# Performance work log

Measured on AMD Instinct MI355X. Metric: run time of the kernel, lower is better.

Reference implementation:

```python
import jax, jax.numpy as jnp
import numpy as np

# Model dims (see init_kwargs)
B, S, D = 2, 2048, 2048          # batch, seq, hidden
H, HD = 16, 128                  # heads, head_dim (= ND + RD)
ND, RD = 64, 64                  # nope dim, rope dim per head
R = 512                          # kv lora rank
THETA = 10000.0


def _rotate_half(x):
    # interleaved rotation: pairs (x0,x1) -> (-x1, x0)
    x1 = x[..., ::2]
    x2 = x[..., 1::2]
    return jnp.stack((-x2, x1), axis=-1).reshape(x.shape)


def apply_rope(x, positions):
    # x: [..., seq, dim]
    dim = x.shape[-1]
    freqs = 1.0 / THETA ** (jnp.arange(0, dim, 2, dtype=x.dtype) / dim)  # [dim/2]
    angles = positions.astype(x.dtype)[:, None] * freqs                  # [seq, dim/2]
    cos = jnp.repeat(jnp.cos(angles), 2, axis=-1)[None, None]            # [1,1,seq,dim]
    sin = jnp.repeat(jnp.sin(angles), 2, axis=-1)[None, None]
    return x * cos + _rotate_half(x) * sin


def setup_inputs() -> dict:
    key = jax.random.key(0)
    ks = jax.random.split(key, 7)
    def lin(k, out_f, in_f):  # torch Linear convention: weight [out, in]
        return jax.random.normal(k, (out_f, in_f), dtype=jnp.float32) * (in_f ** -0.5)
    return {
        "x": jax.random.normal(ks[0], (B, S, D), dtype=jnp.float32),
        "wq": lin(ks[1], D, D),
        "w_kv_down": lin(ks[2], R, D),
        "w_k_up": lin(ks[3], H * ND, R),
        "w_k_rope": lin(ks[4], RD, D),
        "w_v_up": lin(ks[5], D, R),
        "wo": lin(ks[6], D, D),
    }


def reference(x, wq, w_kv_down, w_k_up, w_k_rope, w_v_up, wo):
    b, s, _ = x.shape
    pos = jnp.arange(s)
    scale = 1.0 / np.sqrt(HD).astype(np.float32)

    # queries: [b,H,s,HD] split into nope/rope parts, rope applied per head
    q = (x @ wq.T).reshape(b, s, H, HD).transpose(0, 2, 1, 3)
    q_nope = q[..., :ND]
    q_rope = apply_rope(q[..., ND:], pos)

    # compressed kv latent: [b,s,R]
    c_kv = x @ w_kv_down.T
    k_nope = (c_kv @ w_k_up.T).reshape(b, s, H, ND).transpose(0, 2, 1, 3)  # [b,H,s,ND]
    k_rope = apply_rope((x @ w_k_rope.T)[:, None], pos)[:, 0]             # [b,s,RD], shared across heads
    v = (c_kv @ w_v_up.T).reshape(b, s, H, HD).transpose(0, 2, 1, 3)      # [b,H,s,HD]

    # decomposed scores: nope part (per head) + rope part (shared k)
    scores = jnp.einsum('bhqd,bhkd->bhqk', q_nope, k_nope)
    scores = scores + jnp.einsum('bhqd,bkd->bhqk', q_rope, k_rope)
    scores = scores * scale

    causal = jnp.tril(jnp.ones((s, s), dtype=bool))
    scores = jnp.where(causal[None, None], scores, jnp.finfo(scores.dtype).min)
    attn = jax.nn.softmax(scores, axis=-1)

    out = jnp.einsum('bhqk,bhkd->bhqd', attn, v)
    out = out.transpose(0, 2, 1, 3).reshape(b, s, D)
    return out @ wo.T
```

## Files before the change

kernel.cpp:

```cpp
#include <hip/hip_runtime.h>
#include <stdint.h>


typedef unsigned short u16;
typedef __bf16 bf16x8 __attribute__((ext_vector_type(8)));
typedef float f32x4 __attribute__((ext_vector_type(4)));

#define QLD 2816

__device__ __forceinline__ float bf2f(u16 u) {
    union { unsigned int i; float f; } x; x.i = ((unsigned int)u) << 16; return x.f;
}
__device__ __forceinline__ u16 f2bf(float f) {
    union { float f; unsigned int i; } x; x.f = f;
    unsigned int r = x.i + 0x7fffu + ((x.i >> 16) & 1u);
    return (u16)(r >> 16);
}
__device__ __forceinline__ void store_c(u16* p, float v)  { *p = f2bf(v); }
__device__ __forceinline__ void store_c(float* p, float v){ *p = v; }

#define GLOBAL_AS __attribute__((address_space(1)))
#define LDS_AS    __attribute__((address_space(3)))
__device__ __forceinline__ void gl_lds16(const void* g, void* l) {
    __builtin_amdgcn_global_load_lds((GLOBAL_AS const void*)g, (LDS_AS void*)l, 16, 0, 0);
}

#if __has_builtin(__builtin_amdgcn_exp2f)
__device__ __forceinline__ float exp2fast(float x) { return __builtin_amdgcn_exp2f(x); }
#else
__device__ __forceinline__ float exp2fast(float x) { return __expf(x * 0.6931471805599453f); }
#endif

template<int CTRL>
__device__ __forceinline__ float fmax_dpp(float v) {
    int s = __builtin_bit_cast(int, v);
    int t = __builtin_amdgcn_update_dpp(s, s, CTRL, 0xF, 0xF, true);
    return fmaxf(v, __builtin_bit_cast(float, t));
}
__device__ __forceinline__ float rowmax16(float v) {
    v = fmax_dpp<0xB1>(v);
    v = fmax_dpp<0x4E>(v);
    v = fmax_dpp<0x124>(v);
    v = fmax_dpp<0x128>(v);
    return v;
}

__device__ __forceinline__ void cv8(const float* __restrict__ src,
                                    u16* __restrict__ dst, int i) {
    const float4* s = (const float4*)src;
    float4 v0 = s[2*i], v1 = s[2*i + 1];
    union { u16 u[8]; uint4 v; } o;
    o.u[0] = f2bf(v0.x); o.u[1] = f2bf(v0.y); o.u[2] = f2bf(v0.z); o.u[3] = f2bf(v0.w);
    o.u[4] = f2bf(v1.x); o.u[5] = f2bf(v1.y); o.u[6] = f2bf(v1.z); o.u[7] = f2bf(v1.w);
    *((uint4*)(dst + 8*i)) = o.v;
}

__global__ void convert_all(const float* __restrict__ s_x,
                            const float* __restrict__ s_wq,
                            const float* __restrict__ s_kvd,
                            const float* __restrict__ s_kup,
                            const float* __restrict__ s_vup,
                            const float* __restrict__ s_kr,
                            u16* __restrict__ xc, u16* __restrict__ wqcat,
                            u16* __restrict__ kupc, u16* __restrict__ vupc) {
    int i = blockIdx.x * 256 + threadIdx.x;
    if      (i < 1048576) cv8(s_x,   xc,                          i);
    else if (i < 1572864) cv8(s_wq,  wqcat,                       i - 1048576);
    else if (i < 1703936) cv8(s_kvd, wqcat + (size_t)2112*2048,   i - 1572864);
    else if (i < 1769472) cv8(s_kup, kupc,                        i - 1703936);
    else if (i < 1900544) cv8(s_vup, vupc,                        i - 1769472);
    else if (i < 1916928) cv8(s_kr,  wqcat + (size_t)2048*2048,   i - 1900544);
}

template<int BM, int BN, int EPI, typename CT>
__global__ __launch_bounds__((BM/64)*(BN/64)*64)
void gemm_bt(const u16* __restrict__ A, const u16* __restrict__ W,
             CT* __restrict__ C, int M, int N, int K,
             int lda, int ldw, int ldc) {
    constexpr int BK = 32;
    constexpr int NWAVE = (BM/64)*(BN/64);
    constexpr int NT = NWAVE * 64;
    __shared__ u16 As[BM*BK];
    __shared__ u16 Bs[BN*BK];
    const int tid  = threadIdx.x;
    const int lane = tid & 63, l15 = lane & 15, quad = lane >> 4;
    const int wave = tid >> 6;
    const int wm = wave % (BM/64);
    const int wn = wave / (BM/64);
    const int bm = blockIdx.y * BM;
    const int bn = blockIdx.x * BN;

    const f32x4 fzero = {0.f, 0.f, 0.f, 0.f};
    f32x4 acc[4][4];
    #pragma unroll
    for (int i = 0; i < 4; ++i)
        #pragma unroll
        for (int j = 0; j < 4; ++j) acc[i][j] = fzero;

    const size_t Ab = (size_t)lda * 2;
    const size_t Wb = (size_t)ldw * 2;

    for (int k0 = 0; k0 < K; k0 += BK) {
        #pragma unroll
        for (int i = 0; i < (BM*64)/(NT*16); ++i) {
            int o = (tid + i*NT) * 16;
            int row = o >> 6, colb = o & 63;
            gl_lds16((const char*)A + (size_t)(bm + row)*Ab + (size_t)k0*2 + colb,
                     (char*)As + o);
        }
        #pragma unroll
        for (int i = 0; i < (BN*64)/(NT*16); ++i) {
            int o = (tid + i*NT) * 16;
            int row = o >> 6, colb = o & 63;
            gl_lds16((const char*)W + (size_t)(bn + row)*Wb + (size_t)k0*2 + colb,
                     (char*)Bs + o);
        }
        __syncthreads();

        bf16x8 af[4], bfv[4];
        #pragma unroll
        for (int mt = 0; mt < 4; ++mt)
            af[mt] = *reinterpret_cast<const bf16x8*>(&As[(wm*64 + mt*16 + l15)*BK + quad*8]);
        #pragma unroll
        for (int nt = 0; nt < 4; ++nt)
            bfv[nt] = *reinterpret_cast<const bf16x8*>(&Bs[(wn*64 + nt*16 + l15)*BK + quad*8]);
        #pragma unroll
        for (int mt = 0; mt < 4; ++mt)
            #pragma unroll
            for (int nt = 0; nt < 4; ++nt)
                acc[mt][nt] = __builtin_amdgcn_mfma_f32_16x16x32_bf16(
                    af[mt], bfv[nt], acc[mt][nt], 0, 0, 0);
        __syncthreads();
    }

    #pragma unroll
    for (int mt = 0; mt < 4; ++mt)
        #pragma unroll
        for (int nt = 0; nt < 4; ++nt)
            #pragma unroll
            for (int r = 0; r < 4; ++r) {
                int gm = bm + wm*64 + mt*16 + quad*4 + r;
                int gn = bn + wn*64 + nt*16 + l15;
                size_t ci;
                if (EPI == 1) ci = (size_t)gm*ldc + ((gn >> 6)*128 + (gn & 63));
                else          ci = (size_t)gm*ldc + gn;
                store_c(&C[ci], acc[mt][nt][r]);
            }
}

template<typename CT>
__global__ __launch_bounds__(512, 2)
void gemm256(const u16* __restrict__ A, const u16* __restrict__ W,
             CT* __restrict__ C, int K, int lda, int ldw, int ldc) {
    __shared__ u16 lds[4][16384];
    const int tid  = threadIdx.x;
    const int lane = tid & 63, l15 = lane & 15, quad = lane >> 4;
    const int wave = tid >> 6;
    const int wr = wave >> 2, wc = wave & 3;
    const int bm = blockIdx.y * 256;
    const int bn = blockIdx.x * 256;

    const int R = tid >> 2, slot = tid & 3;
    const int k16 = slot ^ ((R >> 1) & 3);
    const u16* asrc = A + (size_t)(bm + R) * lda + k16 * 8;
    const u16* bsrc = W + (size_t)(bn + R) * ldw + k16 * 8;
    const size_t astep = (size_t)128 * lda;
    const size_t bstep = (size_t)128 * ldw;

    #define STAGE256(st, bi) { \
        const u16* a0_ = asrc + (size_t)(st) * 32; \
        const u16* b0_ = bsrc + (size_t)(st) * 32; \
        gl_lds16(a0_,         &lds[bi][tid * 8]); \
        gl_lds16(a0_ + astep, &lds[bi][(tid + 512) * 8]); \
        gl_lds16(b0_,         &lds[bi][(tid + 1024) * 8]); \
        gl_lds16(b0_ + bstep, &lds[bi][(tid + 1536) * 8]); \
    }

    const f32x4 fzero = {0.f, 0.f, 0.f, 0.f};
    f32x4 acc[8][4];
    #pragma unroll
    for (int i = 0; i < 8; ++i)
        #pragma unroll
        for (int j = 0; j < 4; ++j) acc[i][j] = fzero;

    const int aswz = (quad ^ ((l15 >> 1) & 3)) * 8;

    const int nst = K >> 5;
    STAGE256(0, 0)
    STAGE256(1, 1)
    STAGE256(2, 2)
    asm volatile("s_waitcnt vmcnt(8)" ::: "memory");
    __builtin_amdgcn_s_barrier();

    for (int t = 0; t < nst; ++t) {
        const u16* buf = lds[t & 3];
        bf16x8 af[8], bfv[4];
        #pragma unroll
        for (int mf = 0; mf < 8; ++mf)
            af[mf] = *reinterpret_cast<const bf16x8*>(
                &buf[(wr*128 + mf*16 + l15)*32 + aswz]);
        #pragma unroll
        for (int nf = 0; nf < 4; ++nf)
            bfv[nf] = *reinterpret_cast<const bf16x8*>(
                &buf[8192 + (wc*64 + nf*16 + l15)*32 + aswz]);
        int st = t + 3; if (st > nst - 1) st = nst - 1;
        STAGE256(st, (t + 3) & 3)
        __builtin_amdgcn_s_setprio(1);
        #pragma unroll
        for (int mf = 0; mf < 8; ++mf)
            #pragma unroll
            for (int nf = 0; nf < 4; ++nf)
                acc[mf][nf] = __builtin_amdgcn_mfma_f32_16x16x32_bf16(
                    af[mf], bfv[nf], acc[mf][nf], 0, 0, 0);
        __builtin_amdgcn_s_setprio(0);
        asm volatile("s_waitcnt vmcnt(8) lgkmcnt(0)" ::: "memory");
        __builtin_amdgcn_sched_barrier(0);
        __builtin_amdgcn_s_barrier();
        __builtin_amdgcn_sched_barrier(0);
    }
    #undef STAGE256

    #pragma unroll
    for (int mf = 0; mf < 8; ++mf)
        #pragma unroll
        for (int nf = 0; nf < 4; ++nf)
            #pragma unroll
            for (int r = 0; r < 4; ++r) {
                int gm = bm + wr*128 + mf*16 + quad*4 + r;
                int gn = bn + wc*64 + nf*16 + l15;
                store_c(&C[(size_t)gm * ldc + gn], acc[mf][nf][r]);
            }
}

template<typename CT>
__global__ __launch_bounds__(512, 4)
void gemm128(const u16* __restrict__ A, const u16* __restrict__ W,
             CT* __restrict__ C, int K, int lda, int ldw, int ldc) {
    __shared__ u16 lds[3][12288];
    const int tid  = threadIdx.x;
    const int lane = tid & 63, l15 = lane & 15, quad = lane >> 4;
    const int wave = tid >> 6;
    const int wr = wave >> 2, wc = wave & 3;
    const int bm = blockIdx.y * 128;
    const int bn = blockIdx.x * 256;

    const int R = tid >> 2, slot = tid & 3;
    const int k16 = slot ^ ((R >> 1) & 3);
    const u16* asrc = A + (size_t)(bm + R) * lda + k16 * 8;
    const u16* bsrc = W + (size_t)(bn + R) * ldw + k16 * 8;
    const size_t bstep = (size_t)128 * ldw;

    #define STAGE128(st, bi) { \
        const u16* a0_ = asrc + (size_t)(st) * 32; \
        const u16* b0_ = bsrc + (size_t)(st) * 32; \
        gl_lds16(a0_,         &lds[bi][tid * 8]); \
        gl_lds16(b0_,         &lds[bi][(tid + 512) * 8]); \
        gl_lds16(b0_ + bstep, &lds[bi][(tid + 1024) * 8]); \
    }

    const f32x4 fzero = {0.f, 0.f, 0.f, 0.f};
    f32x4 acc[4][4];
    #pragma unroll
    for (int i = 0; i < 4; ++i)
        #pragma unroll
        for (int j = 0; j < 4; ++j) acc[i][j] = fzero;

    const int aswz = (quad ^ ((l15 >> 1) & 3)) * 8;

    const int nst = K >> 5;
    STAGE128(0, 0)
    STAGE128(1, 1)
    asm volatile("s_waitcnt vmcnt(3)" ::: "memory");
    __builtin_amdgcn_s_barrier();

    int b0 = 0, bs = 2;
    for (int t = 0; t < nst; ++t) {
        const u16* buf = lds[b0];
        bf16x8 af[4], bfv[4];
        #pragma unroll
        for (int mf = 0; mf < 4; ++mf)
            af[mf] = *reinterpret_cast<const bf16x8*>(
                &buf[(wr*64 + mf*16 + l15)*32 + aswz]);
        #pragma unroll
        for (int nf = 0; nf < 4; ++nf)
            bfv[nf] = *reinterpret_cast<const bf16x8*>(
                &buf[4096 + (wc*64 + nf*16 + l15)*32 + aswz]);
        int st = t + 2; if (st > nst - 1) st = nst - 1;
        STAGE128(st, bs)
        __builtin_amdgcn_s_setprio(1);
        #pragma unroll
        for (int mf = 0; mf < 4; ++mf)
            #pragma unroll
            for (int nf = 0; nf < 4; ++nf)
                acc[mf][nf] = __builtin_amdgcn_mfma_f32_16x16x32_bf16(
                    af[mf], bfv[nf], acc[mf][nf], 0, 0, 0);
        __builtin_amdgcn_s_setprio(0);
        asm volatile("s_waitcnt vmcnt(3) lgkmcnt(0)" ::: "memory");
        __builtin_amdgcn_sched_barrier(0);
        __builtin_amdgcn_s_barrier();
        __builtin_amdgcn_sched_barrier(0);
        b0 = (b0 == 2) ? 0 : b0 + 1;
        bs = (bs == 2) ? 0 : bs + 1;
    }
    #undef STAGE128

    #pragma unroll
    for (int mf = 0; mf < 4; ++mf)
        #pragma unroll
        for (int nf = 0; nf < 4; ++nf)
            #pragma unroll
            for (int r = 0; r < 4; ++r) {
                int gm = bm + wr*64 + mf*16 + quad*4 + r;
                int gn = bn + wc*64 + nf*16 + l15;
                store_c(&C[(size_t)gm * ldc + gn], acc[mf][nf][r]);
            }
}

__global__ void rope_woc(u16* __restrict__ qcat, u16* __restrict__ keff,
                         const float* __restrict__ wo_src, u16* __restrict__ woc) {
    const int blk = blockIdx.x;
    if (blk >= 512) {
        int i = (blk - 512) * 256 + threadIdx.x;
        cv8(wo_src, woc, i);
        return;
    }
    int idx = blk * 256 + threadIdx.x;
    int i = idx & 31, r = idx >> 5;
    int pos = r & 2047;
    float freq = powf(10000.0f, -(float)i * (1.0f/32.0f));
    float ang  = (float)pos * freq;
    float s = sinf(ang), c = cosf(ang);

    u16* row = qcat + (size_t)r * QLD + 64 + 2*i;
    #pragma unroll
    for (int h = 0; h < 16; ++h) {
        unsigned int* p = (unsigned int*)(row + h*128);
        unsigned int v = *p;
        float x0 = bf2f((u16)(v & 0xffffu)), x1 = bf2f((u16)(v >> 16));
        unsigned int lo = f2bf(x0*c - x1*s);
        unsigned int hi = f2bf(x1*c + x0*s);
        *p = lo | (hi << 16);
    }

    const u16* p = qcat + (size_t)r * QLD + 2048 + 2*i;
    float x0 = bf2f(p[0]), x1 = bf2f(p[1]);
    union { u16 u[2]; unsigned int w; } o;
    o.u[0] = f2bf(x0*c - x1*s);
    o.u[1] = f2bf(x1*c + x0*s);
    unsigned int* base = (unsigned int*)(keff + (size_t)r*2048 + 64 + 2*i);
    #pragma unroll
    for (int h = 0; h < 16; ++h) base[h*64] = o.w;
}

__global__ __launch_bounds__(256, 3)
void attn_kernel(u16* __restrict__ qcat, const u16* __restrict__ KE,
                 const u16* __restrict__ VT) {
    constexpr int S = 2048;
    const int L = (int)blockIdx.y * 16 + (int)blockIdx.x;
    const int xcd = L & 7, j = L >> 3;
    const int bh   = xcd * 4 + (j & 3);
    const int pair = j >> 2;
    const int b = bh >> 4, h = bh & 15;

    __shared__ u16 Ks[64*128];
    __shared__ u16 Vs[128*64];
    __shared__ u16 Ps[64*68];

    const int tid  = threadIdx.x;
    const int lane = tid & 63, l15 = lane & 15, quad = lane >> 4;
    const int wave = tid >> 6;

    const u16* ksrc[4];
    const u16* vsrc[4];
    #pragma unroll
    for (int i = 0; i < 4; ++i) {
        int g = tid + i*256;
        {
            int r = g >> 4, slot = g & 15, cg = slot ^ (r & 15);
            ksrc[i] = KE + (size_t)(b*S + r)*2048 + h*128 + cg*8;
        }
        {
            int d = g >> 3, slot = g & 7, cg = slot ^ (d & 7);
            vsrc[i] = VT + (size_t)(h*128 + d)*4096 + (size_t)(b*S) + cg*8;
        }
    }

    bf16x8 kreg[4], vreg[4];
    #pragma unroll
    for (int i = 0; i < 4; ++i) {
        kreg[i] = *reinterpret_cast<const bf16x8*>(ksrc[i]);
        vreg[i] = *reinterpret_cast<const bf16x8*>(vsrc[i]);
    }

    union { u16 u[8]; bf16x8 v; } onesu;
    #pragma unroll
    for (int i = 0; i < 8; ++i) onesu.u[i] = 0x3f80;
    const bf16x8 ones = onesu.v;

    const f32x4 fzero = {0.f, 0.f, 0.f, 0.f};
    const float NEG = -1e30f;
    const float KLOG = 0.12751739f;
    const float THR = 8.0f;

    __bf16* PsB = reinterpret_cast<__bf16*>(Ps);

    for (int half = 0; half < 2; ++half) {
        const int qt = half ? pair : 31 - pair;
        const int nkt = qt + 1;

        u16* qbase = qcat + (size_t)(b*S + qt*64) * QLD + h*128;
        bf16x8 aq[4];
        #pragma unroll
        for (int ks = 0; ks < 4; ++ks)
            aq[ks] = *reinterpret_cast<const bf16x8*>(
                qbase + (size_t)(wave*16 + l15)*QLD + ks*32 + quad*8);

        float m2[4]  = {NEG, NEG, NEG, NEG};
        float l_i[4] = {0.f, 0.f, 0.f, 0.f};
        f32x4 oacc[8];
        #pragma unroll
        for (int i = 0; i < 8; ++i) oacc[i] = fzero;

        const int qrow0 = qt*64 + wave*16 + quad*4;

        for (int kt = 0; kt < nkt; ++kt) {
            const bool is_last = (kt == nkt - 1);
            #pragma unroll
            for (int i = 0; i < 4; ++i) {
                *reinterpret_cast<bf16x8*>(&Ks[(tid + i*256) * 8]) = kreg[i];
                *reinterpret_cast<bf16x8*>(&Vs[(tid + i*256) * 8]) = vreg[i];
            }
            {
                int ktn = (kt + 1 < nkt) ? kt + 1 : 0;
                #pragma unroll
                for (int i = 0; i < 4; ++i) {
                    kreg[i] = *reinterpret_cast<const bf16x8*>(ksrc[i] + (size_t)ktn*(64*2048));
                    vreg[i] = *reinterpret_cast<const bf16x8*>(vsrc[i] + (size_t)ktn*64);
                }
            }
            __syncthreads();

            f32x4 sfr[4];
            __builtin_amdgcn_s_setprio(1);
            #pragma unroll
            for (int nt = 0; nt < 4; ++nt) {
                f32x4 s = fzero;
                int n = nt*16 + l15;
                #pragma unroll
                for (int ks = 0; ks < 4; ++ks) {
                    int c = ks*4 + quad;
                    bf16x8 bk = *reinterpret_cast<const bf16x8*>(&Ks[n*128 + ((c ^ l15) * 8)]);
                    s = __builtin_amdgcn_mfma_f32_16x16x32_bf16(aq[ks], bk, s, 0, 0, 0);
                }
                sfr[nt] = s;
            }
            __builtin_amdgcn_s_setprio(0);
            if (is_last) {
                #pragma unroll
                for (int nt = 0; nt < 4; ++nt) {
                    int kg = kt*64 + nt*16 + l15;
                    #pragma unroll
                    for (int r = 0; r < 4; ++r)
                        if (kg > qrow0 + r) sfr[nt][r] = NEG;
                }
            }
            float rm[4];
            #pragma unroll
            for (int r = 0; r < 4; ++r) {
                rm[r] = fmaxf(fmaxf(sfr[0][r], sfr[1][r]), fmaxf(sfr[2][r], sfr[3][r]));
                rm[r] = rowmax16(rm[r]);
            }
            float c2[4];
            int need = 0;
            #pragma unroll
            for (int r = 0; r < 4; ++r) {
                c2[r] = rm[r] * KLOG;
                need |= (c2[r] > m2[r] + THR) ? 1 : 0;
            }
            if (__any(need)) {
                float alpha[4];
                #pragma unroll
                for (int r = 0; r < 4; ++r) {
                    float mn = fmaxf(m2[r], c2[r]);
                    alpha[r] = exp2fast(m2[r] - mn);
                    m2[r] = mn;
                    l_i[r] *= alpha[r];
                }
                #pragma unroll
                for (int i = 0; i < 8; ++i)
                    #pragma unroll
                    for (int r = 0; r < 4; ++r)
                        oacc[i][r] *= alpha[r];
            }
            float pf[4][4];
            #pragma unroll
            for (int nt = 0; nt < 4; ++nt)
                #pragma unroll
                for (int r = 0; r < 4; ++r)
                    pf[nt][r] = exp2fast(__builtin_fmaf(sfr[nt][r], KLOG, -m2[r]));

            #pragma unroll
            for (int nt = 0; nt < 4; ++nt) {
                int base = (wave*16 + quad*4)*68 + nt*16 + l15;
                #pragma unroll
                for (int r = 0; r < 4; ++r)
                    PsB[base + r*68] = (__bf16)pf[nt][r];
            }

            f32x4 lfr = fzero;
            __builtin_amdgcn_s_setprio(1);
            #pragma unroll
            for (int ks = 0; ks < 2; ++ks) {
                bf16x8 pa = *reinterpret_cast<const bf16x8*>(
                    &Ps[(wave*16 + l15)*68 + ks*32 + quad*8]);
                lfr = __builtin_amdgcn_mfma_f32_16x16x32_bf16(pa, ones, lfr, 0, 0, 0);
                #pragma unroll
                for (int ntv = 0; ntv < 8; ++ntv) {
                    int c = ks*4 + quad;
                    bf16x8 bv = *reinterpret_cast<const bf16x8*>(
                        &Vs[(ntv*16 + l15)*64 + ((c ^ (l15 & 7)) * 8)]);
                    oacc[ntv] = __builtin_amdgcn_mfma_f32_16x16x32_bf16(pa, bv, oacc[ntv], 0, 0, 0);
                }
            }
            __builtin_amdgcn_s_setprio(0);
            #pragma unroll
            for (int r = 0; r < 4; ++r) l_i[r] += lfr[r];
            __syncthreads();
        }

        #pragma unroll
        for (int r = 0; r < 4; ++r) {
            float inv = 1.0f / l_i[r];
            int qrow = wave*16 + quad*4 + r;
            #pragma unroll
            for (int ntv = 0; ntv < 8; ++ntv) {
                int d = ntv*16 + l15;
                qbase[(size_t)qrow*QLD + d] = f2bf(oacc[ntv][r] * inv);
            }
        }
    }
}

extern "C" void kernel_launch(void* const* d_in, const int* in_sizes, int n_in,
                              void* d_out, int out_size, void* d_ws, size_t ws_size,
                              hipStream_t stream) {
    (void)in_sizes; (void)n_in; (void)out_size; (void)ws_size;
    float* out = (float*)d_out;
    char* ws = (char*)d_ws;

    u16* xc     = (u16*)(ws);
    u16* qcat   = (u16*)(ws + 16777216);
    u16* keff   = (u16*)(ws + 39845888);
    u16* wqcat  = (u16*)(ws + 56623104);
    u16* kupc   = (u16*)(ws + 68157440);
    u16* vupc   = (u16*)(ws + 69206016);
    u16* vT     = xc;
    u16* woc    = wqcat;

    convert_all<<<7488, 256, 0, stream>>>(
        (const float*)d_in[0], (const float*)d_in[1], (const float*)d_in[2],
        (const float*)d_in[3], (const float*)d_in[5], (const float*)d_in[4],
        xc, wqcat, kupc, vupc);

    gemm256<u16><<<dim3(11, 16), 512, 0, stream>>>(
        xc, wqcat, qcat, 2048, 2048, 2048, QLD);

    rope_woc<<<2560, 256, 0, stream>>>(qcat, keff, (const float*)d_in[6], woc);

    gemm_bt<128,128,1><<<dim3(8, 32), 256, 0, stream>>>(
        qcat + 2112, kupc, keff, 4096, 1024, 512, QLD, 512, 2048);

    gemm128<u16><<<dim3(16, 16), 512, 0, stream>>>(
        vupc, qcat + 2112, vT, 512, 512, QLD, 4096);

    attn_kernel<<<dim3(16, 32), 256, 0, stream>>>(qcat, keff, vT);

    gemm128<float><<<dim3(8, 32), 512, 0, stream>>>(
        qcat, woc, out, 2048, QLD, 2048, 2048);
}
```

Before: 315.2 us.

## Merge k_up and v_up GEMMs into one launch using pipelined gemm128 body

Replaces the simple unpipelined gemm_bt used for the k_nope up-projection with the pipelined gemm128 body, which gains a strided epilogue option. Both up-projection GEMMs (k_up into keff and v_up into vT) now run as one kernel with 384 blocks split by block index. This removes a launch and the tail between the two GEMMs, and the k GEMM gets the faster multi-buffered mainloop. The cost is that each k block now covers a 128x256 tile, so that part runs as fewer, larger blocks.

```diff
diff --git a/kernel.cpp b/kernel.cpp
--- a/kernel.cpp
+++ b/kernel.cpp
@@ -72,82 +72,6 @@
     else if (i < 1916928) cv8(s_kr,  wqcat + (size_t)2048*2048,   i - 1900544);
 }
 
-template<int BM, int BN, int EPI, typename CT>
-__global__ __launch_bounds__((BM/64)*(BN/64)*64)
-void gemm_bt(const u16* __restrict__ A, const u16* __restrict__ W,
-             CT* __restrict__ C, int M, int N, int K,
-             int lda, int ldw, int ldc) {
-    constexpr int BK = 32;
-    constexpr int NWAVE = (BM/64)*(BN/64);
-    constexpr int NT = NWAVE * 64;
-    __shared__ u16 As[BM*BK];
-    __shared__ u16 Bs[BN*BK];
-    const int tid  = threadIdx.x;
-    const int lane = tid & 63, l15 = lane & 15, quad = lane >> 4;
-    const int wave = tid >> 6;
-    const int wm = wave % (BM/64);
-    const int wn = wave / (BM/64);
-    const int bm = blockIdx.y * BM;
-    const int bn = blockIdx.x * BN;
-
-    const f32x4 fzero = {0.f, 0.f, 0.f, 0.f};
-    f32x4 acc[4][4];
-    #pragma unroll
-    for (int i = 0; i < 4; ++i)
-        #pragma unroll
-        for (int j = 0; j < 4; ++j) acc[i][j] = fzero;
-
-    const size_t Ab = (size_t)lda * 2;
-    const size_t Wb = (size_t)ldw * 2;
-
-    for (int k0 = 0; k0 < K; k0 += BK) {
-        #pragma unroll
-        for (int i = 0; i < (BM*64)/(NT*16); ++i) {
-            int o = (tid + i*NT) * 16;
-            int row = o >> 6, colb = o & 63;
-            gl_lds16((const char*)A + (size_t)(bm + row)*Ab + (size_t)k0*2 + colb,
-                     (char*)As + o);
-        }
-        #pragma unroll
-        for (int i = 0; i < (BN*64)/(NT*16); ++i) {
-            int o = (tid + i*NT) * 16;
-            int row = o >> 6, colb = o & 63;
-            gl_lds16((const char*)W + (size_t)(bn + row)*Wb + (size_t)k0*2 + colb,
-                     (char*)Bs + o);
-        }
-        __syncthreads();
-
-        bf16x8 af[4], bfv[4];
-        #pragma unroll
-        for (int mt = 0; mt < 4; ++mt)
-            af[mt] = *reinterpret_cast<const bf16x8*>(&As[(wm*64 + mt*16 + l15)*BK + quad*8]);
-        #pragma unroll
-        for (int nt = 0; nt < 4; ++nt)
-            bfv[nt] = *reinterpret_cast<const bf16x8*>(&Bs[(wn*64 + nt*16 + l15)*BK + quad*8]);
-        #pragma unroll
-        for (int mt = 0; mt < 4; ++mt)
-            #pragma unroll
-            for (int nt = 0; nt < 4; ++nt)
-                acc[mt][nt] = __builtin_amdgcn_mfma_f32_16x16x32_bf16(
-                    af[mt], bfv[nt], acc[mt][nt], 0, 0, 0);
-        __syncthreads();
-    }
-
-    #pragma unroll
-    for (int mt = 0; mt < 4; ++mt)
-        #pragma unroll
-        for (int nt = 0; nt < 4; ++nt)
-            #pragma unroll
-            for (int r = 0; r < 4; ++r) {
-                int gm = bm + wm*64 + mt*16 + quad*4 + r;
-                int gn = bn + wn*64 + nt*16 + l15;
-                size_t ci;
-                if (EPI == 1) ci = (size_t)gm*ldc + ((gn >> 6)*128 + (gn & 63));
-                else          ci = (size_t)gm*ldc + gn;
-                store_c(&C[ci], acc[mt][nt][r]);
-            }
-}
-
 template<typename CT>
 __global__ __launch_bounds__(512, 2)
 void gemm256(const u16* __restrict__ A, const u16* __restrict__ W,
@@ -232,17 +156,16 @@
             }
 }
 
-template<typename CT>
-__global__ __launch_bounds__(512, 4)
-void gemm128(const u16* __restrict__ A, const u16* __restrict__ W,
-             CT* __restrict__ C, int K, int lda, int ldw, int ldc) {
-    __shared__ u16 lds[3][12288];
+template<int EPI, typename CT>
+__device__ __forceinline__ void gemm128_body(
+        u16 (*lds)[12288],
+        const u16* __restrict__ A, const u16* __restrict__ W,
+        CT* __restrict__ C, int K, int lda, int ldw, int ldc,
+        int bm, int bn) {
     const int tid  = threadIdx.x;
     const int lane = tid & 63, l15 = lane & 15, quad = lane >> 4;
     const int wave = tid >> 6;
     const int wr = wave >> 2, wc = wave & 3;
-    const int bm = blockIdx.y * 128;
-    const int bn = blockIdx.x * 256;
 
     const int R = tid >> 2, slot = tid & 3;
     const int k16 = slot ^ ((R >> 1) & 3);
@@ -312,8 +235,36 @@
             for (int r = 0; r < 4; ++r) {
                 int gm = bm + wr*64 + mf*16 + quad*4 + r;
                 int gn = bn + wc*64 + nf*16 + l15;
-                store_c(&C[(size_t)gm * ldc + gn], acc[mf][nf][r]);
-            }
+                size_t ci;
+                if (EPI == 1) ci = (size_t)gm*ldc + ((gn >> 6)*128 + (gn & 63));
+                else          ci = (size_t)gm*ldc + gn;
+                store_c(&C[ci], acc[mf][nf][r]);
+            }
+}
+
+template<typename CT>
+__global__ __launch_bounds__(512, 4)
+void gemm128(const u16* __restrict__ A, const u16* __restrict__ W,
+             CT* __restrict__ C, int K, int lda, int ldw, int ldc) {
+    __shared__ u16 lds[3][12288];
+    gemm128_body<0>(lds, A, W, C, K, lda, ldw, ldc,
+                    (int)blockIdx.y * 128, (int)blockIdx.x * 256);
+}
+
+__global__ __launch_bounds__(512, 4)
+void kv_up(const u16* __restrict__ ckv, const u16* __restrict__ kupc,
+           u16* __restrict__ keff, const u16* __restrict__ vupc,
+           u16* __restrict__ vT) {
+    __shared__ u16 lds[3][12288];
+    const int bx = blockIdx.x;
+    if (bx < 128) {
+        int bn = (bx & 3) * 256, bm = (bx >> 2) * 128;
+        gemm128_body<1>(lds, ckv, kupc, keff, 512, QLD, 512, 2048, bm, bn);
+    } else {
+        int b2 = bx - 128;
+        int bn = (b2 & 15) * 256, bm = (b2 >> 4) * 128;
+        gemm128_body<0>(lds, vupc, ckv, vT, 512, 512, QLD, 4096, bm, bn);
+    }
 }
 
 __global__ void rope_woc(u16* __restrict__ qcat, u16* __restrict__ keff,
@@ -567,11 +518,7 @@
 
     rope_woc<<<2560, 256, 0, stream>>>(qcat, keff, (const float*)d_in[6], woc);
 
-    gemm_bt<128,128,1><<<dim3(8, 32), 256, 0, stream>>>(
-        qcat + 2112, kupc, keff, 4096, 1024, 512, QLD, 512, 2048);
-
-    gemm128<u16><<<dim3(16, 16), 512, 0, stream>>>(
-        vupc, qcat + 2112, vT, 512, 512, QLD, 4096);
+    kv_up<<<384, 512, 0, stream>>>(qcat + 2112, kupc, keff, vupc, vT);
 
     attn_kernel<<<dim3(16, 32), 256, 0, stream>>>(qcat, keff, vT);
 
```

After: 310.5 us. About the same (-1.5%).
